# Performance work log

Measured on AMD Instinct MI355X. Metric: run time of the kernel, lower is better.

Reference implementation:

```python
import jax, jax.numpy as jnp
import numpy as np

E, T = 8, 256          # n_experts, chunk length
IN, OUT = 1024, 1024   # input_size, output_size
D1, D2 = 32, 32        # nearest factors of IN
DO1, DO2 = 32, 32      # nearest factors of OUT
B, L = 8, 2048
LOSS_COEF = 1e-5


def setup_inputs() -> dict:
    key = jax.random.key(0)
    ks = jax.random.split(key, 12)
    eyeE = lambda d, k: (jnp.broadcast_to(jnp.eye(d, dtype=jnp.float32), (E, d, d))
                         + 0.01 * jax.random.normal(k, (E, d, d), jnp.float32))
    return {
        "x": jax.random.normal(ks[0], (B, L, IN), jnp.float32),
        "w_gate": 0.02 * jax.random.normal(ks[1], (IN, E), jnp.float32),
        "weight": 0.02 * jax.random.normal(ks[2], (E, OUT, IN), jnp.float32),
        "bias": 0.02 * jax.random.normal(ks[3], (E, OUT), jnp.float32),
        "res_weight": 0.02 * jax.random.normal(ks[4], (OUT, IN), jnp.float32),
        "res_bias": 0.02 * jax.random.normal(ks[5], (1, OUT), jnp.float32),
        "curve1_in": eyeE(D1, ks[6]),
        "curve2_in": eyeE(D2, ks[7]),
        "curve1_out": eyeE(DO1, ks[8]),
        "curve2_out": eyeE(DO2, ks[9]),
        "curve1_bias": eyeE(DO1, ks[10]),
        "curve2_bias": eyeE(DO2, ks[11]),
    }


def _cv_squared(v):
    v = v.astype(jnp.float32)
    return jnp.var(v, ddof=1) / (jnp.mean(v) ** 2 + 1e-10)


def reference(x, w_gate, weight, bias, res_weight, res_bias,
              curve1_in, curve2_in, curve1_out, curve2_out,
              curve1_bias, curve2_bias):
    Bx, Lx, d = x.shape
    N = Lx // T
    BN = Bx * N
    xr = x.reshape(BN, T, d)

    # --- gating (eval mode, ties_merging forces k = n_experts -> plain softmax) ---
    logits = xr.mean(axis=1) @ w_gate            # [BN, E]
    gates = jax.nn.softmax(logits, axis=1)        # [BN, E]
    load = (gates > 0).sum(axis=0).astype(jnp.float32)
    importance = gates.sum(axis=0)
    loss = (_cv_squared(importance) + _cv_squared(load)) * LOSS_COEF

    # --- roll gates by one segment, keeping each sample's first chunk (detached) ---
    e_first = jax.lax.stop_gradient(gates.reshape(Bx, N, E)[:, 0])
    g = jnp.roll(gates, 1, axis=0).reshape(Bx, N, E)
    g = g.at[:, 0].set(e_first).reshape(BN, E)

    # --- Kronecker curve-factored expert weight merge ---
    rw = (weight - res_weight).reshape(E, DO1, DO2, D1, D2)
    rw = jnp.einsum('bij,bjklm->biklm', curve1_out, rw)
    rw = jnp.einsum('bik,bjklm->bjilm', curve2_out, rw)
    rw = jnp.einsum('bil,bjklm->bjkim', curve1_in, rw)
    rw = jnp.einsum('bim,bjklm->bjkli', curve2_in, rw)
    rw = rw.reshape(E, OUT, IN)
    expert_weights = res_weight + jnp.einsum('be,eoi->boi', g, rw)  # [BN, O, I]

    y = jnp.einsum('bij,bkj->bik', xr, expert_weights)  # [BN, T, O]

    # --- curve-factored expert bias merge ---
    rb = (bias - res_bias).reshape(E, DO1, DO2)
    rb = jnp.einsum('bki,bij->bkj', curve1_bias, rb)      # [E, DO1, DO2]
    rb = jnp.einsum('bkj,bij->bik', curve2_bias, rb)      # [E, DO1, DO2]
    rb = rb.reshape(E, OUT)
    expert_bias = res_bias + jnp.einsum('be,eo->bo', g, rb)  # [BN, O]

    y = (y + expert_bias[:, None, :]).reshape(Bx, Lx, OUT)
    return y, loss
```

## Files before the change

### kernel.cpp

```cpp
#include <hip/hip_runtime.h>
#include <cstdint>

typedef __bf16 bf16x8 __attribute__((ext_vector_type(8)));
typedef float  f32x4  __attribute__((ext_vector_type(4)));
typedef unsigned int u32x4 __attribute__((ext_vector_type(4)));
using u16 = unsigned short;

struct alignas(8) u16x4 { u16 x, y, z, w; };

__device__ __forceinline__ u16 f2bf(float f) {
  unsigned u = __builtin_bit_cast(unsigned, f);
  u = (u + 0x7FFFu + ((u >> 16) & 1u)) >> 16;
  return (u16)u;
}
__device__ __forceinline__ float bf2f(u16 u) {
  unsigned v = ((unsigned)u) << 16;
  return __builtin_bit_cast(float, v);
}

static constexpr size_t OFF_XBF  = 0;
static constexpr size_t OFF_EW   = 33554432;
static constexpr size_t OFF_T2   = 33554432;
static constexpr size_t OFF_PM   = 67108864;
static constexpr size_t OFF_RW   = 167772160;
static constexpr size_t OFF_LG   = 201326592;
static constexpr size_t OFF_G    = 201588736;
static constexpr size_t OFF_RB   = 201592832;
static constexpr size_t WS_NEED  = 201887744;

__global__ __launch_bounds__(256) void k_means(const float* __restrict__ x,
                                               float* __restrict__ pm,
                                               u16* __restrict__ xbf) {
  int b = blockIdx.x, q = blockIdx.y, tid = threadIdx.x;
  const float* xb = x + (size_t)b * 262144 + (size_t)q * 16384 + tid * 4;
  u16* xo = xbf + (size_t)b * 262144 + (size_t)q * 16384 + tid * 4;
  float s0 = 0.f, s1 = 0.f, s2 = 0.f, s3 = 0.f;
#pragma unroll
  for (int t = 0; t < 16; ++t) {
    float4 v = *(const float4*)(xb + t * 1024);
    s0 += v.x; s1 += v.y; s2 += v.z; s3 += v.w;
    u16x4 o; o.x = f2bf(v.x); o.y = f2bf(v.y); o.z = f2bf(v.z); o.w = f2bf(v.w);
    *(u16x4*)(xo + t * 1024) = o;
  }
  float4 sv; sv.x = s0; sv.y = s1; sv.z = s2; sv.w = s3;
  *(float4*)(pm + ((size_t)b * 16 + q) * 1024 + tid * 4) = sv;
}

__global__ __launch_bounds__(256) void k_mergeA(const float* __restrict__ W,
                                                const float* __restrict__ R,
                                                const float* __restrict__ c1o,
                                                const float* __restrict__ c2o,
                                                u16* __restrict__ T2t,
                                                const float* __restrict__ pm,
                                                const float* __restrict__ w_gate,
                                                float* __restrict__ logits,
                                                const float* __restrict__ bias,
                                                const float* __restrict__ res_bias,
                                                const float* __restrict__ c1b,
                                                const float* __restrict__ c2b,
                                                float* __restrict__ rb) {
  int e = blockIdx.y, bx = blockIdx.x, tid = threadIdx.x;
  if (bx == 128) {
    __shared__ float red[4][8];
    for (int c = 0; c < 8; ++c) {
      int b = e * 8 + c;
      const float* p = pm + (size_t)b * 16384 + tid * 4;
      float4 s = {0.f, 0.f, 0.f, 0.f};
#pragma unroll
      for (int q = 0; q < 16; ++q) {
        float4 v = *(const float4*)(p + q * 1024);
        s.x += v.x; s.y += v.y; s.z += v.z; s.w += v.w;
      }
      int i0 = tid * 4;
      float acc[8];
#pragma unroll
      for (int e2 = 0; e2 < 8; ++e2) {
        acc[e2] = s.x * w_gate[(i0 + 0) * 8 + e2] + s.y * w_gate[(i0 + 1) * 8 + e2]
                + s.z * w_gate[(i0 + 2) * 8 + e2] + s.w * w_gate[(i0 + 3) * 8 + e2];
      }
#pragma unroll
      for (int off = 32; off >= 1; off >>= 1)
#pragma unroll
        for (int e2 = 0; e2 < 8; ++e2) acc[e2] += __shfl_down(acc[e2], off, 64);
      if ((tid & 63) == 0)
#pragma unroll
        for (int e2 = 0; e2 < 8; ++e2) red[tid >> 6][e2] = acc[e2];
      __syncthreads();
      if (tid < 8)
        logits[b * 8 + tid] =
            (red[0][tid] + red[1][tid] + red[2][tid] + red[3][tid]) * (1.f / 256.f);
      __syncthreads();
    }
    __shared__ float rb0[32][33], rb1[32][33], m1b[32][32], m2b[32][32];
    for (int idx = tid; idx < 1024; idx += 256) {
      int i = idx >> 5, j = idx & 31;
      rb0[i][j] = bias[e * 1024 + idx] - res_bias[idx];
      m1b[i][j] = c1b[e * 1024 + idx];
      m2b[i][j] = c2b[e * 1024 + idx];
    }
    __syncthreads();
    for (int idx = tid; idx < 1024; idx += 256) {
      int p = idx >> 5, j = idx & 31;
      float s = 0.f;
#pragma unroll
      for (int i = 0; i < 32; ++i) s += m1b[p][i] * rb0[i][j];
      rb1[p][j] = s;
    }
    __syncthreads();
    for (int idx = tid; idx < 1024; idx += 256) {
      int p = idx >> 5, q = idx & 31;
      float s = 0.f;
#pragma unroll
      for (int j = 0; j < 32; ++j) s += m2b[q][j] * rb1[p][j];
      rb[e * 1024 + idx] = s;
    }
    return;
  }
  __shared__ float dw[8 * 1024];
  __shared__ float m1[1024], m2[1024];
  int c0 = bx * 8;
  const float* We = W + (size_t)e * 1048576;
  for (int idx = tid; idx < 1024; idx += 256) {
    m1[idx] = c1o[e * 1024 + idx];
    m2[idx] = c2o[e * 1024 + idx];
  }
  {
    int r = tid >> 1, h = (tid & 1) * 4;
#pragma unroll
    for (int i = 0; i < 8; ++i) {
      int row = r + i * 128;
      const float4 wv = *(const float4*)(We + (size_t)row * 1024 + c0 + h);
      const float4 rv = *(const float4*)(R + (size_t)row * 1024 + c0 + h);
      dw[(h + 0) * 1024 + row] = wv.x - rv.x;
      dw[(h + 1) * 1024 + row] = wv.y - rv.y;
      dw[(h + 2) * 1024 + row] = wv.z - rv.z;
      dw[(h + 3) * 1024 + row] = wv.w - rv.w;
    }
  }
  __syncthreads();
  int i1 = tid & 31, c = tid >> 5;
  const float* dwc = dw + c * 1024;
  float U[32];
#pragma unroll
  for (int k = 0; k < 32; ++k) U[k] = 0.f;
  for (int j = 0; j < 32; ++j) {
    float cj = m1[i1 * 32 + j];
    const float4* rowp = (const float4*)(dwc + j * 32);
#pragma unroll
    for (int k4 = 0; k4 < 8; ++k4) {
      float4 v = rowp[k4];
      U[k4 * 4 + 0] += cj * v.x; U[k4 * 4 + 1] += cj * v.y;
      U[k4 * 4 + 2] += cj * v.z; U[k4 * 4 + 3] += cj * v.w;
    }
  }
  u16* obase = T2t + (size_t)e * 1048576 + (size_t)(c0 + c) * 1024 + i1 * 32;
#pragma unroll
  for (int g4 = 0; g4 < 8; ++g4) {
    float s[4];
#pragma unroll
    for (int q = 0; q < 4; ++q) {
      const float4* m2r = (const float4*)(m2 + (g4 * 4 + q) * 32);
      float acc = 0.f;
#pragma unroll
      for (int k4 = 0; k4 < 8; ++k4) {
        float4 mv = m2r[k4];
        acc += mv.x * U[k4 * 4 + 0] + mv.y * U[k4 * 4 + 1]
             + mv.z * U[k4 * 4 + 2] + mv.w * U[k4 * 4 + 3];
      }
      s[q] = acc;
    }
    u16x4 o4; o4.x = f2bf(s[0]); o4.y = f2bf(s[1]); o4.z = f2bf(s[2]); o4.w = f2bf(s[3]);
    *(u16x4*)(obase + g4 * 4) = o4;
  }
}

__global__ __launch_bounds__(256) void k_mergeB(const u16* __restrict__ T2t,
                                                const float* __restrict__ c1i,
                                                const float* __restrict__ c2i,
                                                u16* __restrict__ RWbf,
                                                const float* __restrict__ logits,
                                                float* __restrict__ g,
                                                float* __restrict__ loss_out) {
  int e = blockIdx.y, bx = blockIdx.x, tid = threadIdx.x;
  if (bx == 128) {
    if (e != 0) return;
    __shared__ float gates[64][8];
    __shared__ float imp[8];
    if (tid < 64) {
      float lg[8];
#pragma unroll
      for (int j = 0; j < 8; ++j) lg[j] = logits[tid * 8 + j];
      float mx = lg[0];
#pragma unroll
      for (int j = 1; j < 8; ++j) mx = fmaxf(mx, lg[j]);
      float s = 0.f, ex[8];
#pragma unroll
      for (int j = 0; j < 8; ++j) { ex[j] = expf(lg[j] - mx); s += ex[j]; }
      float inv = 1.f / s;
#pragma unroll
      for (int j = 0; j < 8; ++j) gates[tid][j] = ex[j] * inv;
    }
    __syncthreads();
    if (tid < 8) {
      float s = 0.f;
      for (int bb = 0; bb < 64; ++bb) s += gates[bb][tid];
      imp[tid] = s;
    }
    __syncthreads();
    if (tid == 0) {
      float mean = 0.f;
#pragma unroll
      for (int j = 0; j < 8; ++j) mean += imp[j];
      mean *= (1.f / 8.f);
      float var = 0.f;
#pragma unroll
      for (int j = 0; j < 8; ++j) { float d = imp[j] - mean; var += d * d; }
      var *= (1.f / 7.f);
      loss_out[0] = (var / (mean * mean + 1e-10f)) * 1e-5f;
    }
    __syncthreads();
    if (tid < 64) {
      int src = ((tid & 7) == 0) ? tid : tid - 1;
#pragma unroll
      for (int j = 0; j < 8; ++j) g[tid * 8 + j] = gates[src][j];
    }
    return;
  }
  __shared__ float t2[8 * 1024];
  __shared__ float m1[1024], m2[1024];
  int o0 = bx * 8;
  const u16* Te = T2t + (size_t)e * 1048576;
  for (int idx = tid; idx < 1024; idx += 256) {
    m1[idx] = c1i[e * 1024 + idx];
    m2[idx] = c2i[e * 1024 + idx];
  }
  {
    int r = tid >> 1, h = (tid & 1) * 4;
#pragma unroll
    for (int i = 0; i < 8; ++i) {
      int row = r + i * 128;
      const u16x4 tv = *(const u16x4*)(Te + (size_t)row * 1024 + o0 + h);
      t2[(h + 0) * 1024 + row] = bf2f(tv.x);
      t2[(h + 1) * 1024 + row] = bf2f(tv.y);
      t2[(h + 2) * 1024 + row] = bf2f(tv.z);
      t2[(h + 3) * 1024 + row] = bf2f(tv.w);
    }
  }
  __syncthreads();
  int i1 = tid & 31, oc = tid >> 5;
  const float* t2c = t2 + oc * 1024;
  float A[32];
#pragma unroll
  for (int m = 0; m < 32; ++m) A[m] = 0.f;
  for (int l = 0; l < 32; ++l) {
    float cl = m1[i1 * 32 + l];
    const float4* rowp = (const float4*)(t2c + l * 32);
#pragma unroll
    for (int m4 = 0; m4 < 8; ++m4) {
      float4 v = rowp[m4];
      A[m4 * 4 + 0] += cl * v.x; A[m4 * 4 + 1] += cl * v.y;
      A[m4 * 4 + 2] += cl * v.z; A[m4 * 4 + 3] += cl * v.w;
    }
  }
  u16* obase = RWbf + ((size_t)e * 1024 + o0 + oc) * 1024 + i1 * 32;
#pragma unroll
  for (int g4 = 0; g4 < 8; ++g4) {
    float s[4];
#pragma unroll
    for (int q = 0; q < 4; ++q) {
      const float4* m2r = (const float4*)(m2 + (g4 * 4 + q) * 32);
      float acc = 0.f;
#pragma unroll
      for (int m4 = 0; m4 < 8; ++m4) {
        float4 mv = m2r[m4];
        acc += mv.x * A[m4 * 4 + 0] + mv.y * A[m4 * 4 + 1]
             + mv.z * A[m4 * 4 + 2] + mv.w * A[m4 * 4 + 3];
      }
      s[q] = acc;
    }
    u16x4 o4; o4.x = f2bf(s[0]); o4.y = f2bf(s[1]); o4.z = f2bf(s[2]); o4.w = f2bf(s[3]);
    *(u16x4*)(obase + g4 * 4) = o4;
  }
}

__global__ __launch_bounds__(256) void k_combine(const u16* __restrict__ RWbf,
                                                 const float* __restrict__ R,
                                                 const float* __restrict__ g,
                                                 u16* __restrict__ EW) {
  __shared__ float gs[512];
  int o = blockIdx.x, tid = threadIdx.x;
  for (int idx = tid; idx < 512; idx += 256) gs[idx] = g[idx];
  __syncthreads();
  int i0 = tid * 4;
  float4 r4 = *(const float4*)(R + (size_t)o * 1024 + i0);
  float4 w[8];
#pragma unroll
  for (int e = 0; e < 8; ++e) {
    u16x4 t = *(const u16x4*)(RWbf + (size_t)e * 1048576 + (size_t)o * 1024 + i0);
    w[e].x = bf2f(t.x); w[e].y = bf2f(t.y); w[e].z = bf2f(t.z); w[e].w = bf2f(t.w);
  }
  for (int b = 0; b < 64; ++b) {
    float a0 = r4.x, a1 = r4.y, a2 = r4.z, a3 = r4.w;
#pragma unroll
    for (int e = 0; e < 8; ++e) {
      float ge = gs[b * 8 + e];
      a0 += ge * w[e].x; a1 += ge * w[e].y; a2 += ge * w[e].z; a3 += ge * w[e].w;
    }
    u16x4 u; u.x = f2bf(a0); u.y = f2bf(a1); u.z = f2bf(a2); u.w = f2bf(a3);
    *(u16x4*)(EW + (size_t)b * 1048576 + (size_t)o * 1024 + i0) = u;
  }
}

__global__ __launch_bounds__(1024) void k_gemm(const u16* __restrict__ Xb,
                                               const u16* __restrict__ EW,
                                               const float* __restrict__ rb,
                                               const float* __restrict__ res_b,
                                               const float* __restrict__ g,
                                               float* __restrict__ Y) {
  __shared__ alignas(16) u16 As[2][256 * 64];
  __shared__ alignas(16) u16 Bs[2][256 * 64];
  int hw = blockIdx.x;
  int xcd = hw & 7;
  int b  = xcd * 8 + (hw >> 5);
  int nt = (hw >> 3) & 3;
  int t0 = b * 256, o0 = nt * 256;
  int tid = threadIdx.x, lane = tid & 63, wv = tid >> 6;
  int wr = wv >> 2, wc = wv & 3;
  f32x4 acc[4][4] = {};
  const u16* aG = Xb + (size_t)t0 * 1024;
  const u16* bG = EW + (size_t)b * 1048576 + (size_t)o0 * 1024;
  int srow = tid >> 3;
  int kcol = (tid & 7) << 3;
  int lr = lane & 15;
  int sx = lr & 7;
  u32x4 la[2], lb[2];
#pragma unroll
  for (int iss = 0; iss < 2; ++iss) {
    int r = srow + iss * 128;
    la[iss] = *(const u32x4*)(aG + (size_t)r * 1024 + kcol);
    lb[iss] = *(const u32x4*)(bG + (size_t)r * 1024 + kcol);
  }
  for (int kt = 0; kt < 16; ++kt) {
    int cur = kt & 1;
#pragma unroll
    for (int iss = 0; iss < 2; ++iss) {
      int r = srow + iss * 128;
      int wcl = (((tid & 7) ^ (r & 7)) << 3);
      *(u32x4*)&As[cur][r * 64 + wcl] = la[iss];
      *(u32x4*)&Bs[cur][r * 64 + wcl] = lb[iss];
    }
    __syncthreads();
    if (kt < 15) {
      int k0n = (kt + 1) << 6;
#pragma unroll
      for (int iss = 0; iss < 2; ++iss) {
        int r = srow + iss * 128;
        la[iss] = *(const u32x4*)(aG + (size_t)r * 1024 + k0n + kcol);
        lb[iss] = *(const u32x4*)(bG + (size_t)r * 1024 + k0n + kcol);
      }
    }
#pragma unroll
    for (int kk = 0; kk < 2; ++kk) {
      int c16 = kk * 4 + (lane >> 4);
      int cp = ((c16 ^ sx) << 3);
      bf16x8 af[4], bfr[4];
#pragma unroll
      for (int mi = 0; mi < 4; ++mi)
        af[mi] = *(const bf16x8*)&As[cur][(wr * 64 + mi * 16 + lr) * 64 + cp];
#pragma unroll
      for (int ni = 0; ni < 4; ++ni)
        bfr[ni] = *(const bf16x8*)&Bs[cur][(wc * 64 + ni * 16 + lr) * 64 + cp];
#pragma unroll
      for (int mi = 0; mi < 4; ++mi)
#pragma unroll
        for (int ni = 0; ni < 4; ++ni)
          acc[mi][ni] = __builtin_amdgcn_mfma_f32_16x16x32_bf16(af[mi], bfr[ni], acc[mi][ni], 0, 0, 0);
    }
  }
  float ge[8];
#pragma unroll
  for (int e = 0; e < 8; ++e) ge[e] = g[b * 8 + e];
  int rbase = (lane >> 4) << 2;
#pragma unroll
  for (int ni = 0; ni < 4; ++ni) {
    int o = o0 + wc * 64 + ni * 16 + lr;
    float ebv = res_b[o];
#pragma unroll
    for (int e = 0; e < 8; ++e) ebv += ge[e] * rb[e * 1024 + o];
#pragma unroll
    for (int mi = 0; mi < 4; ++mi) {
      int trow = t0 + wr * 64 + mi * 16 + rbase;
      float* yp = Y + (size_t)trow * 1024 + o;
      yp[0]    = acc[mi][ni][0] + ebv;
      yp[1024] = acc[mi][ni][1] + ebv;
      yp[2048] = acc[mi][ni][2] + ebv;
      yp[3072] = acc[mi][ni][3] + ebv;
    }
  }
}

extern "C" void kernel_launch(void* const* d_in, const int* in_sizes, int n_in,
                              void* d_out, int out_size, void* d_ws, size_t ws_size,
                              hipStream_t stream) {
  const float* x      = (const float*)d_in[0];
  const float* w_gate = (const float*)d_in[1];
  const float* weight = (const float*)d_in[2];
  const float* bias   = (const float*)d_in[3];
  const float* res_w  = (const float*)d_in[4];
  const float* res_b  = (const float*)d_in[5];
  const float* c1i    = (const float*)d_in[6];
  const float* c2i    = (const float*)d_in[7];
  const float* c1o    = (const float*)d_in[8];
  const float* c2o    = (const float*)d_in[9];
  const float* c1b    = (const float*)d_in[10];
  const float* c2b    = (const float*)d_in[11];
  float* y = (float*)d_out;

  if (ws_size < WS_NEED) return;

  char* wsb = (char*)d_ws;
  u16*   xbf   = (u16*)(wsb + OFF_XBF);
  u16*   EW    = (u16*)(wsb + OFF_EW);
  u16*   T2t   = (u16*)(wsb + OFF_T2);
  float* pm    = (float*)(wsb + OFF_PM);
  u16*   RWbf  = (u16*)(wsb + OFF_RW);
  float* lgts  = (float*)(wsb + OFF_LG);
  float* g     = (float*)(wsb + OFF_G);
  float* rb    = (float*)(wsb + OFF_RB);

  k_means   <<<dim3(64, 16), 256, 0, stream>>>(x, pm, xbf);
  k_mergeA  <<<dim3(129, 8), 256, 0, stream>>>(weight, res_w, c1o, c2o, T2t,
                                               pm, w_gate, lgts,
                                               bias, res_b, c1b, c2b, rb);
  k_mergeB  <<<dim3(129, 8), 256, 0, stream>>>(T2t, c1i, c2i, RWbf,
                                               lgts, g, y + 16777216);
  k_combine <<<1024, 256, 0, stream>>>(RWbf, res_w, g, EW);
  k_gemm    <<<256, 1024, 0, stream>>>(xbf, EW, rb, res_b, g, y);
}
```

Baseline: 235.3 us.

## Fuse per-sample expert weight combine into GEMM B-tile loading

Drops the k_combine kernel, which wrote a 64×1024×1024 bf16 per-sample expert weight tensor. The GEMM now builds each B tile itself from the eight per-expert bf16 matrices weighted by the gates. res_weight is folded into each expert's RW so the gates (which sum to one) reconstruct it. The GEMM also moves to 512 threads with 8×4 MFMA tiles per wave and a new block-to-tile mapping, and the logits reduction is split into its own small kernel so it no longer serializes inside mergeA. In exchange, each B tile costs eight times the global reads plus extra ALU work in the GEMM main loop, and folding the residual into the bf16 weights adds rounding error.

```diff
diff --git a/kernel.cpp b/kernel.cpp
--- a/kernel.cpp
+++ b/kernel.cpp
@@ -19,7 +19,6 @@
 }
 
 static constexpr size_t OFF_XBF  = 0;
-static constexpr size_t OFF_EW   = 33554432;
 static constexpr size_t OFF_T2   = 33554432;
 static constexpr size_t OFF_PM   = 67108864;
 static constexpr size_t OFF_RW   = 167772160;
@@ -46,14 +45,44 @@
   *(float4*)(pm + ((size_t)b * 16 + q) * 1024 + tid * 4) = sv;
 }
 
+__global__ __launch_bounds__(256) void k_redlogits(const float* __restrict__ pm,
+                                                   const float* __restrict__ w_gate,
+                                                   float* __restrict__ logits) {
+  __shared__ float red[4][8];
+  int b = blockIdx.x, tid = threadIdx.x;
+  const float* p = pm + (size_t)b * 16384 + tid * 4;
+  float4 s = {0.f, 0.f, 0.f, 0.f};
+#pragma unroll
+  for (int q = 0; q < 16; ++q) {
+    float4 v = *(const float4*)(p + q * 1024);
+    s.x += v.x; s.y += v.y; s.z += v.z; s.w += v.w;
+  }
+  int i0 = tid * 4;
+  float acc[8];
+#pragma unroll
+  for (int e = 0; e < 8; ++e) {
+    acc[e] = s.x * w_gate[(i0 + 0) * 8 + e] + s.y * w_gate[(i0 + 1) * 8 + e]
+           + s.z * w_gate[(i0 + 2) * 8 + e] + s.w * w_gate[(i0 + 3) * 8 + e];
+  }
+#pragma unroll
+  for (int off = 32; off >= 1; off >>= 1)
+#pragma unroll
+    for (int e = 0; e < 8; ++e) acc[e] += __shfl_down(acc[e], off, 64);
+  int wv = tid >> 6;
+  if ((tid & 63) == 0)
+#pragma unroll
+    for (int e = 0; e < 8; ++e) red[wv][e] = acc[e];
+  __syncthreads();
+  if (tid < 8)
+    logits[b * 8 + tid] =
+        (red[0][tid] + red[1][tid] + red[2][tid] + red[3][tid]) * (1.f / 256.f);
+}
+
 __global__ __launch_bounds__(256) void k_mergeA(const float* __restrict__ W,
                                                 const float* __restrict__ R,
                                                 const float* __restrict__ c1o,
                                                 const float* __restrict__ c2o,
                                                 u16* __restrict__ T2t,
-                                                const float* __restrict__ pm,
-                                                const float* __restrict__ w_gate,
-                                                float* __restrict__ logits,
                                                 const float* __restrict__ bias,
                                                 const float* __restrict__ res_bias,
                                                 const float* __restrict__ c1b,
@@ -61,36 +90,6 @@
                                                 float* __restrict__ rb) {
   int e = blockIdx.y, bx = blockIdx.x, tid = threadIdx.x;
   if (bx == 128) {
-    __shared__ float red[4][8];
-    for (int c = 0; c < 8; ++c) {
-      int b = e * 8 + c;
-      const float* p = pm + (size_t)b * 16384 + tid * 4;
-      float4 s = {0.f, 0.f, 0.f, 0.f};
-#pragma unroll
-      for (int q = 0; q < 16; ++q) {
-        float4 v = *(const float4*)(p + q * 1024);
-        s.x += v.x; s.y += v.y; s.z += v.z; s.w += v.w;
-      }
-      int i0 = tid * 4;
-      float acc[8];
-#pragma unroll
-      for (int e2 = 0; e2 < 8; ++e2) {
-        acc[e2] = s.x * w_gate[(i0 + 0) * 8 + e2] + s.y * w_gate[(i0 + 1) * 8 + e2]
-                + s.z * w_gate[(i0 + 2) * 8 + e2] + s.w * w_gate[(i0 + 3) * 8 + e2];
-      }
-#pragma unroll
-      for (int off = 32; off >= 1; off >>= 1)
-#pragma unroll
-        for (int e2 = 0; e2 < 8; ++e2) acc[e2] += __shfl_down(acc[e2], off, 64);
-      if ((tid & 63) == 0)
-#pragma unroll
-        for (int e2 = 0; e2 < 8; ++e2) red[tid >> 6][e2] = acc[e2];
-      __syncthreads();
-      if (tid < 8)
-        logits[b * 8 + tid] =
-            (red[0][tid] + red[1][tid] + red[2][tid] + red[3][tid]) * (1.f / 256.f);
-      __syncthreads();
-    }
     __shared__ float rb0[32][33], rb1[32][33], m1b[32][32], m2b[32][32];
     for (int idx = tid; idx < 1024; idx += 256) {
       int i = idx >> 5, j = idx & 31;
@@ -177,6 +176,7 @@
 __global__ __launch_bounds__(256) void k_mergeB(const u16* __restrict__ T2t,
                                                 const float* __restrict__ c1i,
                                                 const float* __restrict__ c2i,
+                                                const float* __restrict__ R,
                                                 u16* __restrict__ RWbf,
                                                 const float* __restrict__ logits,
                                                 float* __restrict__ g,
@@ -262,6 +262,7 @@
       A[m4 * 4 + 2] += cl * v.z; A[m4 * 4 + 3] += cl * v.w;
     }
   }
+  const float* Rrow = R + (size_t)(o0 + oc) * 1024 + i1 * 32;
   u16* obase = RWbf + ((size_t)e * 1024 + o0 + oc) * 1024 + i1 * 32;
 #pragma unroll
   for (int g4 = 0; g4 < 8; ++g4) {
@@ -269,7 +270,7 @@
 #pragma unroll
     for (int q = 0; q < 4; ++q) {
       const float4* m2r = (const float4*)(m2 + (g4 * 4 + q) * 32);
-      float acc = 0.f;
+      float acc = Rrow[g4 * 4 + q];
 #pragma unroll
       for (int m4 = 0; m4 < 8; ++m4) {
         float4 mv = m2r[m4];
@@ -283,103 +284,100 @@
   }
 }
 
-__global__ __launch_bounds__(256) void k_combine(const u16* __restrict__ RWbf,
-                                                 const float* __restrict__ R,
-                                                 const float* __restrict__ g,
-                                                 u16* __restrict__ EW) {
-  __shared__ float gs[512];
-  int o = blockIdx.x, tid = threadIdx.x;
-  for (int idx = tid; idx < 512; idx += 256) gs[idx] = g[idx];
-  __syncthreads();
-  int i0 = tid * 4;
-  float4 r4 = *(const float4*)(R + (size_t)o * 1024 + i0);
-  float4 w[8];
-#pragma unroll
-  for (int e = 0; e < 8; ++e) {
-    u16x4 t = *(const u16x4*)(RWbf + (size_t)e * 1048576 + (size_t)o * 1024 + i0);
-    w[e].x = bf2f(t.x); w[e].y = bf2f(t.y); w[e].z = bf2f(t.z); w[e].w = bf2f(t.w);
-  }
-  for (int b = 0; b < 64; ++b) {
-    float a0 = r4.x, a1 = r4.y, a2 = r4.z, a3 = r4.w;
-#pragma unroll
-    for (int e = 0; e < 8; ++e) {
-      float ge = gs[b * 8 + e];
-      a0 += ge * w[e].x; a1 += ge * w[e].y; a2 += ge * w[e].z; a3 += ge * w[e].w;
-    }
-    u16x4 u; u.x = f2bf(a0); u.y = f2bf(a1); u.z = f2bf(a2); u.w = f2bf(a3);
-    *(u16x4*)(EW + (size_t)b * 1048576 + (size_t)o * 1024 + i0) = u;
-  }
-}
-
-__global__ __launch_bounds__(1024) void k_gemm(const u16* __restrict__ Xb,
-                                               const u16* __restrict__ EW,
-                                               const float* __restrict__ rb,
-                                               const float* __restrict__ res_b,
-                                               const float* __restrict__ g,
-                                               float* __restrict__ Y) {
+__global__ __launch_bounds__(512) void k_gemm(const u16* __restrict__ Xb,
+                                              const u16* __restrict__ RWbf,
+                                              const float* __restrict__ rb,
+                                              const float* __restrict__ res_b,
+                                              const float* __restrict__ g,
+                                              float* __restrict__ Y) {
   __shared__ alignas(16) u16 As[2][256 * 64];
   __shared__ alignas(16) u16 Bs[2][256 * 64];
   int hw = blockIdx.x;
-  int xcd = hw & 7;
-  int b  = xcd * 8 + (hw >> 5);
-  int nt = (hw >> 3) & 3;
+  int nt = (hw & 7) >> 1;
+  int b  = (hw & 1) * 32 + (hw >> 3);
   int t0 = b * 256, o0 = nt * 256;
   int tid = threadIdx.x, lane = tid & 63, wv = tid >> 6;
   int wr = wv >> 2, wc = wv & 3;
-  f32x4 acc[4][4] = {};
+  f32x4 acc[8][4] = {};
   const u16* aG = Xb + (size_t)t0 * 1024;
-  const u16* bG = EW + (size_t)b * 1048576 + (size_t)o0 * 1024;
+  const u16* bG = RWbf + (size_t)o0 * 1024;
+  float ge[8];
+#pragma unroll
+  for (int e = 0; e < 8; ++e) ge[e] = g[b * 8 + e];
   int srow = tid >> 3;
   int kcol = (tid & 7) << 3;
+  int rB = tid >> 1;
+  int cB0 = (tid & 1) * 32;
+  int gB0 = (tid & 1) * 4;
   int lr = lane & 15;
   int sx = lr & 7;
-  u32x4 la[2], lb[2];
-#pragma unroll
-  for (int iss = 0; iss < 2; ++iss) {
-    int r = srow + iss * 128;
+  u32x4 la[4];
+#pragma unroll
+  for (int iss = 0; iss < 4; ++iss) {
+    int r = srow + iss * 64;
     la[iss] = *(const u32x4*)(aG + (size_t)r * 1024 + kcol);
-    lb[iss] = *(const u32x4*)(bG + (size_t)r * 1024 + kcol);
   }
   for (int kt = 0; kt < 16; ++kt) {
     int cur = kt & 1;
-#pragma unroll
-    for (int iss = 0; iss < 2; ++iss) {
-      int r = srow + iss * 128;
+    int k0 = kt << 6;
+#pragma unroll
+    for (int iss = 0; iss < 4; ++iss) {
+      int r = srow + iss * 64;
       int wcl = (((tid & 7) ^ (r & 7)) << 3);
       *(u32x4*)&As[cur][r * 64 + wcl] = la[iss];
-      *(u32x4*)&Bs[cur][r * 64 + wcl] = lb[iss];
+    }
+    const u16* bRow = bG + (size_t)rB * 1024 + k0 + cB0;
+#pragma unroll
+    for (int q = 0; q < 4; ++q) {
+      float fa[8];
+#pragma unroll
+      for (int j = 0; j < 8; ++j) fa[j] = 0.f;
+#pragma unroll
+      for (int e = 0; e < 8; ++e) {
+        u32x4 v = *(const u32x4*)(bRow + (size_t)e * 1048576 + q * 8);
+        float w = ge[e];
+#pragma unroll
+        for (int h = 0; h < 4; ++h) {
+          unsigned lo = v[h] << 16;
+          unsigned hi = v[h] & 0xFFFF0000u;
+          fa[2 * h]     += w * __builtin_bit_cast(float, lo);
+          fa[2 * h + 1] += w * __builtin_bit_cast(float, hi);
+        }
+      }
+      u32x4 pk;
+#pragma unroll
+      for (int h = 0; h < 4; ++h)
+        pk[h] = (unsigned)f2bf(fa[2 * h]) | ((unsigned)f2bf(fa[2 * h + 1]) << 16);
+      int gq = gB0 + q;
+      *(u32x4*)&Bs[cur][rB * 64 + ((gq ^ (rB & 7)) << 3)] = pk;
     }
     __syncthreads();
     if (kt < 15) {
       int k0n = (kt + 1) << 6;
 #pragma unroll
-      for (int iss = 0; iss < 2; ++iss) {
-        int r = srow + iss * 128;
+      for (int iss = 0; iss < 4; ++iss) {
+        int r = srow + iss * 64;
         la[iss] = *(const u32x4*)(aG + (size_t)r * 1024 + k0n + kcol);
-        lb[iss] = *(const u32x4*)(bG + (size_t)r * 1024 + k0n + kcol);
       }
     }
 #pragma unroll
     for (int kk = 0; kk < 2; ++kk) {
       int c16 = kk * 4 + (lane >> 4);
       int cp = ((c16 ^ sx) << 3);
-      bf16x8 af[4], bfr[4];
-#pragma unroll
-      for (int mi = 0; mi < 4; ++mi)
-        af[mi] = *(const bf16x8*)&As[cur][(wr * 64 + mi * 16 + lr) * 64 + cp];
+      bf16x8 af[8], bfr[4];
+#pragma unroll
+      for (int mi = 0; mi < 8; ++mi)
+        af[mi] = *(const bf16x8*)&As[cur][(wr * 128 + mi * 16 + lr) * 64 + cp];
 #pragma unroll
       for (int ni = 0; ni < 4; ++ni)
         bfr[ni] = *(const bf16x8*)&Bs[cur][(wc * 64 + ni * 16 + lr) * 64 + cp];
 #pragma unroll
-      for (int mi = 0; mi < 4; ++mi)
+      for (int mi = 0; mi < 8; ++mi)
 #pragma unroll
         for (int ni = 0; ni < 4; ++ni)
           acc[mi][ni] = __builtin_amdgcn_mfma_f32_16x16x32_bf16(af[mi], bfr[ni], acc[mi][ni], 0, 0, 0);
     }
   }
-  float ge[8];
-#pragma unroll
-  for (int e = 0; e < 8; ++e) ge[e] = g[b * 8 + e];
   int rbase = (lane >> 4) << 2;
 #pragma unroll
   for (int ni = 0; ni < 4; ++ni) {
@@ -388,8 +386,8 @@
 #pragma unroll
     for (int e = 0; e < 8; ++e) ebv += ge[e] * rb[e * 1024 + o];
 #pragma unroll
-    for (int mi = 0; mi < 4; ++mi) {
-      int trow = t0 + wr * 64 + mi * 16 + rbase;
+    for (int mi = 0; mi < 8; ++mi) {
+      int trow = t0 + wr * 128 + mi * 16 + rbase;
       float* yp = Y + (size_t)trow * 1024 + o;
       yp[0]    = acc[mi][ni][0] + ebv;
       yp[1024] = acc[mi][ni][1] + ebv;
@@ -420,7 +418,6 @@
 
   char* wsb = (char*)d_ws;
   u16*   xbf   = (u16*)(wsb + OFF_XBF);
-  u16*   EW    = (u16*)(wsb + OFF_EW);
   u16*   T2t   = (u16*)(wsb + OFF_T2);
   float* pm    = (float*)(wsb + OFF_PM);
   u16*   RWbf  = (u16*)(wsb + OFF_RW);
@@ -428,12 +425,11 @@
   float* g     = (float*)(wsb + OFF_G);
   float* rb    = (float*)(wsb + OFF_RB);
 
-  k_means   <<<dim3(64, 16), 256, 0, stream>>>(x, pm, xbf);
-  k_mergeA  <<<dim3(129, 8), 256, 0, stream>>>(weight, res_w, c1o, c2o, T2t,
-                                               pm, w_gate, lgts,
-                                               bias, res_b, c1b, c2b, rb);
-  k_mergeB  <<<dim3(129, 8), 256, 0, stream>>>(T2t, c1i, c2i, RWbf,
-                                               lgts, g, y + 16777216);
-  k_combine <<<1024, 256, 0, stream>>>(RWbf, res_w, g, EW);
-  k_gemm    <<<256, 1024, 0, stream>>>(xbf, EW, rb, res_b, g, y);
-}
+  k_means    <<<dim3(64, 16), 256, 0, stream>>>(x, pm, xbf);
+  k_redlogits<<<64, 256, 0, stream>>>(pm, w_gate, lgts);
+  k_mergeA   <<<dim3(129, 8), 256, 0, stream>>>(weight, res_w, c1o, c2o, T2t,
+                                                bias, res_b, c1b, c2b, rb);
+  k_mergeB   <<<dim3(129, 8), 256, 0, stream>>>(T2t, c1i, c2i, res_w, RWbf,
+                                                lgts, g, y + 16777216);
+  k_gemm     <<<256, 512, 0, stream>>>(xbf, RWbf, rb, res_b, g, y);
+}
```

After: 318.0 us. 1.35x slower.
